# Kernel optimization log

Hardware: AMD Instinct MI355X
Metric: run time of the kernel (lower is better)

## Reference

```python
import jax, jax.numpy as jnp
import numpy as np

N = 16_777_216
NUM_BINS = 5
TAIL_BOUND = 2.5


def setup_inputs() -> dict:
    key = jax.random.key(0)
    kx, kp = jax.random.split(key)
    x = jax.random.normal(kx, (N, 1), dtype=jnp.float32)
    # nn.Parameter(torch.randn(3*K+1) * 0.01)
    params = jax.random.normal(kp, (3 * NUM_BINS + 1,), dtype=jnp.float32) * 0.01
    return {"x": x, "params": params}


def _rqs_forward(xs, params, tail_bound):
    K = (params.shape[0] - 1) // 3
    widths, heights, derivs = params[:K], params[K : 2 * K], params[2 * K :]
    # Params are shared across all rows, so softmax/cumsum are tiny 1-D ops.
    W = jax.nn.softmax(widths) * (2 * tail_bound)           # [K]
    H = jax.nn.softmax(heights) * (2 * tail_bound)          # [K]
    D = jax.nn.softplus(derivs) + 1e-5                      # [K+1]
    cum_w = jnp.concatenate([jnp.full((1,), -tail_bound, W.dtype), -tail_bound + jnp.cumsum(W)])  # [K+1]
    cum_h = jnp.concatenate([jnp.full((1,), -tail_bound, H.dtype), -tail_bound + jnp.cumsum(H)])  # [K+1]

    inside = (xs >= -tail_bound) & (xs <= tail_bound)
    x_safe = jnp.where(inside, xs, 0.0)
    # torch.searchsorted(right=False) == jnp.searchsorted(side='left')
    bin_idx = jnp.clip(jnp.searchsorted(cum_w[1:-1], x_safe), 0, K - 1)  # [N]

    x_k, x_k1 = cum_w[bin_idx], cum_w[bin_idx + 1]
    y_k, y_k1 = cum_h[bin_idx], cum_h[bin_idx + 1]
    d_k, d_k1 = D[bin_idx], D[bin_idx + 1]
    s_k = H[bin_idx] / W[bin_idx]

    xi = jnp.clip((x_safe - x_k) / (x_k1 - x_k + 1e-8), 0.0, 1.0)
    one_m_xi = 1.0 - xi
    denom = s_k + (d_k + d_k1 - 2.0 * s_k) * xi * one_m_xi
    z_inside = y_k + (y_k1 - y_k) * (s_k * xi * xi + d_k * xi * one_m_xi) / (denom + 1e-8)
    log_jac_inside = (
        2.0 * jnp.log(s_k + 1e-8)
        + jnp.log(d_k1 * xi * xi + 2.0 * s_k * xi * one_m_xi + d_k * one_m_xi * one_m_xi + 1e-8)
        - 2.0 * jnp.log(jnp.abs(denom) + 1e-8)
    )

    z = jnp.where(inside, z_inside, xs)
    log_jac = jnp.where(inside, log_jac_inside, 0.0)
    return z, log_jac


def reference(x, params):
    xs = x[:, 0]  # squeeze(-1)
    z, lj = _rqs_forward(xs, params, TAIL_BOUND)
    return z[:, None], lj
```

## Files before the change

kernel.cpp:

```cpp
#include <hip/hip_runtime.h>
#include <math.h>

#define NN 16777216
#define KBINS 5
#define TBOUND 2.5f


__device__ __forceinline__ void rqs1(float x,
                                     float c1, float c2, float c3, float c4,
                                     const float4* __restrict__ t0,
                                     const float4* __restrict__ t1,
                                     float& z, float& lj) {
    bool inside = (x >= -TBOUND) && (x <= TBOUND);
    float xs = inside ? x : 0.0f;
    int b = (int)(xs > c1) + (int)(xs > c2) + (int)(xs > c3) + (int)(xs > c4);
    float4 a  = t0[b];
    float4 cc = t1[b];
    float xi = (xs - a.x) * a.y;
    xi = fminf(fmaxf(xi, 0.0f), 1.0f);
    float omxi = 1.0f - xi;
    float xo   = xi * omxi;
    float sk = a.z;
    float dk = cc.z, dk1 = cc.w;
    float denom = fmaf(dk + dk1 - 2.0f * sk, xo, sk);
    float num   = fmaf(sk * xi, xi, dk * xo);
    float zin   = fmaf(cc.y, num / (denom + 1e-8f), cc.x);
    float numj  = fmaf(dk1 * xi, xi, fmaf(2.0f * sk, xo, dk * omxi * omxi));
    float ljin  = a.w + __logf(numj + 1e-8f) - 2.0f * __logf(fabsf(denom) + 1e-8f);
    z  = inside ? zin  : x;
    lj = inside ? ljin : 0.0f;
}

__global__ __launch_bounds__(256) void rqs_kernel(const float* __restrict__ x,
                                                  const float* __restrict__ params,
                                                  float* __restrict__ out) {
    __shared__ float4 t0[KBINS];
    __shared__ float4 t1[KBINS];
    __shared__ float  cwS[KBINS + 1];

    if (threadIdx.x == 0) {
        float p[3 * KBINS + 1];
        #pragma unroll
        for (int i = 0; i < 3 * KBINS + 1; ++i) p[i] = params[i];

        float mw = p[0];
        #pragma unroll
        for (int i = 1; i < KBINS; ++i) mw = fmaxf(mw, p[i]);
        float ew[KBINS]; float sw = 0.0f;
        #pragma unroll
        for (int i = 0; i < KBINS; ++i) { ew[i] = __expf(p[i] - mw); sw += ew[i]; }
        float W[KBINS];
        #pragma unroll
        for (int i = 0; i < KBINS; ++i) W[i] = ew[i] / sw * (2.0f * TBOUND);

        float mh = p[KBINS];
        #pragma unroll
        for (int i = 1; i < KBINS; ++i) mh = fmaxf(mh, p[KBINS + i]);
        float eh[KBINS]; float sh = 0.0f;
        #pragma unroll
        for (int i = 0; i < KBINS; ++i) { eh[i] = __expf(p[KBINS + i] - mh); sh += eh[i]; }
        float H[KBINS];
        #pragma unroll
        for (int i = 0; i < KBINS; ++i) H[i] = eh[i] / sh * (2.0f * TBOUND);

        float D[KBINS + 1];
        #pragma unroll
        for (int i = 0; i < KBINS + 1; ++i) {
            float v = p[2 * KBINS + i];
            D[i] = fmaxf(v, 0.0f) + log1pf(__expf(-fabsf(v))) + 1e-5f;
        }

        float cw[KBINS + 1], ch[KBINS + 1];
        cw[0] = -TBOUND; ch[0] = -TBOUND;
        float aw = 0.0f, ah = 0.0f;
        #pragma unroll
        for (int i = 0; i < KBINS; ++i) {
            aw += W[i]; cw[i + 1] = -TBOUND + aw;
            ah += H[i]; ch[i + 1] = -TBOUND + ah;
        }

        #pragma unroll
        for (int b = 0; b < KBINS; ++b) {
            float sk = H[b] / W[b];
            t0[b] = make_float4(cw[b],
                                1.0f / (cw[b + 1] - cw[b] + 1e-8f),
                                sk,
                                2.0f * logf(sk + 1e-8f));
            t1[b] = make_float4(ch[b], ch[b + 1] - ch[b], D[b], D[b + 1]);
        }
        #pragma unroll
        for (int i = 0; i < KBINS + 1; ++i) cwS[i] = cw[i];
    }
    __syncthreads();

    float c1 = cwS[1], c2 = cwS[2], c3 = cwS[3], c4 = cwS[4];

    const float4* __restrict__ xv  = (const float4*)x;
    float4* __restrict__ zv  = (float4*)out;
    float4* __restrict__ ljv = (float4*)(out + NN);

    const int nvec   = NN / 4;
    const int tid    = blockIdx.x * blockDim.x + threadIdx.x;
    const int stride = gridDim.x * blockDim.x;

    for (int i = tid; i < nvec; i += stride) {
        float4 xx = xv[i];
        float4 zo, lo;
        rqs1(xx.x, c1, c2, c3, c4, t0, t1, zo.x, lo.x);
        rqs1(xx.y, c1, c2, c3, c4, t0, t1, zo.y, lo.y);
        rqs1(xx.z, c1, c2, c3, c4, t0, t1, zo.z, lo.z);
        rqs1(xx.w, c1, c2, c3, c4, t0, t1, zo.w, lo.w);
        zv[i]  = zo;
        ljv[i] = lo;
    }
}

extern "C" void kernel_launch(void* const* d_in, const int* in_sizes, int n_in,
                              void* d_out, int out_size, void* d_ws, size_t ws_size,
                              hipStream_t stream) {
    const float* x      = (const float*)d_in[0];
    const float* params = (const float*)d_in[1];
    float* out          = (float*)d_out;
    dim3 grid(2048), block(256);
    rqs_kernel<<<grid, block, 0, stream>>>(x, params, out);
}
```

Before: 185.8 us.

## Batch all loads up front with nontemporal access and use hardware rcp/log

Replaces the grid-stride loop with a fixed 8-iteration unrolled loop that issues all eight vector loads before any compute, raising memory-level parallelism. Loads and stores use nontemporal builtins to bypass cache retention for this streaming workload. The divide and log calls are replaced with raw hardware rcp and log2 intrinsics, with a ln2 scale applied afterwards. The code now hardcodes the grid size so that it covers N exactly, and it uses more registers.

```diff
diff --git a/kernel.cpp b/kernel.cpp
--- a/kernel.cpp
+++ b/kernel.cpp
@@ -5,17 +5,22 @@
 #define KBINS 5
 #define TBOUND 2.5f
 
+#define NBLOCKS 2048
+#define NTHREADS 256
+#define ITERS 8
 
-__device__ __forceinline__ void rqs1(float x,
-                                     float c1, float c2, float c3, float c4,
-                                     const float4* __restrict__ t0,
-                                     const float4* __restrict__ t1,
-                                     float& z, float& lj) {
+typedef float f32x4 __attribute__((ext_vector_type(4)));
+
+
+__device__ __forceinline__ float2 rqs1(float x,
+                                       float c1, float c2, float c3, float c4,
+                                       const f32x4* __restrict__ t0,
+                                       const f32x4* __restrict__ t1) {
     bool inside = (x >= -TBOUND) && (x <= TBOUND);
     float xs = inside ? x : 0.0f;
     int b = (int)(xs > c1) + (int)(xs > c2) + (int)(xs > c3) + (int)(xs > c4);
-    float4 a  = t0[b];
-    float4 cc = t1[b];
+    f32x4 a  = t0[b];
+    f32x4 cc = t1[b];
     float xi = (xs - a.x) * a.y;
     xi = fminf(fmaxf(xi, 0.0f), 1.0f);
     float omxi = 1.0f - xi;
@@ -24,19 +29,23 @@
     float dk = cc.z, dk1 = cc.w;
     float denom = fmaf(dk + dk1 - 2.0f * sk, xo, sk);
     float num   = fmaf(sk * xi, xi, dk * xo);
-    float zin   = fmaf(cc.y, num / (denom + 1e-8f), cc.x);
+    float zin   = fmaf(cc.y * num, __builtin_amdgcn_rcpf(denom + 1e-8f), cc.x);
     float numj  = fmaf(dk1 * xi, xi, fmaf(2.0f * sk, xo, dk * omxi * omxi));
-    float ljin  = a.w + __logf(numj + 1e-8f) - 2.0f * __logf(fabsf(denom) + 1e-8f);
-    z  = inside ? zin  : x;
-    lj = inside ? ljin : 0.0f;
+    float l1 = __builtin_amdgcn_logf(numj + 1e-8f);
+    float l2 = __builtin_amdgcn_logf(fabsf(denom) + 1e-8f);
+    float ljin = fmaf(0.69314718056f, fmaf(-2.0f, l2, l1), a.w);
+    float2 r;
+    r.x = inside ? zin  : x;
+    r.y = inside ? ljin : 0.0f;
+    return r;
 }
 
-__global__ __launch_bounds__(256) void rqs_kernel(const float* __restrict__ x,
-                                                  const float* __restrict__ params,
-                                                  float* __restrict__ out) {
-    __shared__ float4 t0[KBINS];
-    __shared__ float4 t1[KBINS];
-    __shared__ float  cwS[KBINS + 1];
+__global__ __launch_bounds__(NTHREADS) void rqs_kernel(const float* __restrict__ x,
+                                                       const float* __restrict__ params,
+                                                       float* __restrict__ out) {
+    __shared__ f32x4 t0[KBINS];
+    __shared__ f32x4 t1[KBINS];
+    __shared__ float cwS[KBINS + 1];
 
     if (threadIdx.x == 0) {
         float p[3 * KBINS + 1];
@@ -82,11 +91,10 @@
         #pragma unroll
         for (int b = 0; b < KBINS; ++b) {
             float sk = H[b] / W[b];
-            t0[b] = make_float4(cw[b],
-                                1.0f / (cw[b + 1] - cw[b] + 1e-8f),
-                                sk,
-                                2.0f * logf(sk + 1e-8f));
-            t1[b] = make_float4(ch[b], ch[b + 1] - ch[b], D[b], D[b + 1]);
+            f32x4 v0 = { cw[b], 1.0f / (cw[b + 1] - cw[b] + 1e-8f), sk, 2.0f * logf(sk + 1e-8f) };
+            f32x4 v1 = { ch[b], ch[b + 1] - ch[b], D[b], D[b + 1] };
+            t0[b] = v0;
+            t1[b] = v1;
         }
         #pragma unroll
         for (int i = 0; i < KBINS + 1; ++i) cwS[i] = cw[i];
@@ -95,23 +103,29 @@
 
     float c1 = cwS[1], c2 = cwS[2], c3 = cwS[3], c4 = cwS[4];
 
-    const float4* __restrict__ xv  = (const float4*)x;
-    float4* __restrict__ zv  = (float4*)out;
-    float4* __restrict__ ljv = (float4*)(out + NN);
+    const f32x4* __restrict__ xv  = (const f32x4*)x;
+    f32x4* __restrict__ zv  = (f32x4*)out;
+    f32x4* __restrict__ ljv = (f32x4*)(out + NN);
 
-    const int nvec   = NN / 4;
     const int tid    = blockIdx.x * blockDim.x + threadIdx.x;
-    const int stride = gridDim.x * blockDim.x;
+    const int stride = NBLOCKS * NTHREADS;
 
-    for (int i = tid; i < nvec; i += stride) {
-        float4 xx = xv[i];
-        float4 zo, lo;
-        rqs1(xx.x, c1, c2, c3, c4, t0, t1, zo.x, lo.x);
-        rqs1(xx.y, c1, c2, c3, c4, t0, t1, zo.y, lo.y);
-        rqs1(xx.z, c1, c2, c3, c4, t0, t1, zo.z, lo.z);
-        rqs1(xx.w, c1, c2, c3, c4, t0, t1, zo.w, lo.w);
-        zv[i]  = zo;
-        ljv[i] = lo;
+    f32x4 xx[ITERS];
+    #pragma unroll
+    for (int k = 0; k < ITERS; ++k)
+        xx[k] = __builtin_nontemporal_load(xv + tid + k * stride);
+
+    #pragma unroll
+    for (int k = 0; k < ITERS; ++k) {
+        int i = tid + k * stride;
+        float2 r0 = rqs1(xx[k].x, c1, c2, c3, c4, t0, t1);
+        float2 r1 = rqs1(xx[k].y, c1, c2, c3, c4, t0, t1);
+        float2 r2 = rqs1(xx[k].z, c1, c2, c3, c4, t0, t1);
+        float2 r3 = rqs1(xx[k].w, c1, c2, c3, c4, t0, t1);
+        f32x4 zo = { r0.x, r1.x, r2.x, r3.x };
+        f32x4 lo = { r0.y, r1.y, r2.y, r3.y };
+        __builtin_nontemporal_store(zo, zv + i);
+        __builtin_nontemporal_store(lo, ljv + i);
     }
 }
 
@@ -121,6 +135,5 @@
     const float* x      = (const float*)d_in[0];
     const float* params = (const float*)d_in[1];
     float* out          = (float*)d_out;
-    dim3 grid(2048), block(256);
-    rqs_kernel<<<grid, block, 0, stream>>>(x, params, out);
+    rqs_kernel<<<dim3(NBLOCKS), dim3(NTHREADS), 0, stream>>>(x, params, out);
 }
```

Result: no change. 187.2 us (+0.8%).
